# Performance work log

Hardware: AMD Instinct MI355X
Metric: run time of the kernel (lower is better)

## Reference

```python
import jax, jax.numpy as jnp
import numpy as np

NEG_SLOPE = 0.2


def gat_conv(x, edge_index, W, a_src, a_dst, b, concat):
    """PyG-style GATConv: add self-loops, linear, edge attention, scatter-softmax, scatter-add."""
    N = x.shape[0]
    H, C = a_src.shape
    loop = jnp.arange(N)
    src = jnp.concatenate([edge_index[0], loop])  # source j (messages flow j -> i)
    dst = jnp.concatenate([edge_index[1], loop])  # target i (aggregation node)
    h = (x @ W).reshape(N, H, C)                  # [N,H,C]
    alpha_s = jnp.sum(h * a_src, axis=-1)         # [N,H]
    alpha_d = jnp.sum(h * a_dst, axis=-1)         # [N,H]
    e = jax.nn.leaky_relu(alpha_s[src] + alpha_d[dst], NEG_SLOPE)  # [E,H]
    # numerically stable scatter-softmax over edges grouped by destination node
    m = jax.ops.segment_max(e, dst, num_segments=N)                # [N,H]
    ex = jnp.exp(e - m[dst])
    denom = jax.ops.segment_sum(ex, dst, num_segments=N)           # [N,H]
    alpha = ex / (denom[dst] + 1e-16)                              # [E,H]
    out = jax.ops.segment_sum(h[src] * alpha[:, :, None], dst, num_segments=N)  # [N,H,C]
    out = out.reshape(N, H * C) if concat else out.mean(axis=1)
    return out + b


def setup_inputs() -> dict:
    key = jax.random.key(0)
    ks = jax.random.split(key, 12)
    N, E, F_IN, HID, OUT, HEADS = 100000, 1600000, 128, 128, 64, 4
    C1 = HID // HEADS
    x = jax.random.normal(ks[0], (N, F_IN), dtype=jnp.float32)
    edge_index = jax.random.randint(ks[1], (2, E), 0, N, dtype=jnp.int64)
    s = 0.05
    return {
        "x": x,
        "edge_index": edge_index,
        "W1": jax.random.normal(ks[2], (F_IN, HEADS * C1), dtype=jnp.float32) * s,
        "a_src1": jax.random.normal(ks[3], (HEADS, C1), dtype=jnp.float32) * s,
        "a_dst1": jax.random.normal(ks[4], (HEADS, C1), dtype=jnp.float32) * s,
        "b1": jnp.zeros((HEADS * C1,), dtype=jnp.float32),
        "W2": jax.random.normal(ks[5], (HID, OUT), dtype=jnp.float32) * s,
        "a_src2": jax.random.normal(ks[6], (1, OUT), dtype=jnp.float32) * s,
        "a_dst2": jax.random.normal(ks[7], (1, OUT), dtype=jnp.float32) * s,
        "b2": jnp.zeros((OUT,), dtype=jnp.float32),
    }


def reference(x, edge_index, W1, a_src1, a_dst1, b1, W2, a_src2, a_dst2, b2):
    h = jax.nn.elu(gat_conv(x, edge_index, W1, a_src1, a_dst1, b1, concat=True))
    # F.dropout(p=0.5, training=False) is the identity in eval mode
    out = gat_conv(h, edge_index, W2, a_src2, a_dst2, b2, concat=False)
    return out
```

## Files before the change

### kernel.cpp

```cpp
#include <hip/hip_runtime.h>
#include <hip/hip_fp16.h>
#include <math.h>
#include <string.h>


#define BSH 9
#define DPB 512
#define NBK 256
#define CH1 16384
#define DBINS 512
#define HB 128
#define LOG2E 1.44269504088896f

using half8 = __attribute__((ext_vector_type(8))) _Float16;
using half4 = __attribute__((ext_vector_type(4))) _Float16;
using floatx4 = __attribute__((ext_vector_type(4))) float;

__device__ __forceinline__ float exp2_fast(float x) {
#if __has_builtin(__builtin_amdgcn_exp2f)
    return __builtin_amdgcn_exp2f(x);
#else
    return exp2f(x);
#endif
}

__device__ __forceinline__ void wfrag(const float* __restrict__ W, __half* __restrict__ WtF,
                                      int NC, int fid) {
    int col = fid & 15, quad = (fid >> 4) & 3, rest = fid >> 6;
    int NT = NC >> 4;
    int t = rest & (NT - 1), k0s = rest / NT;
    int n = t * 16 + col;
    int k = k0s * 32 + quad * 8;
#pragma unroll
    for (int j = 0; j < 8; ++j)
        WtF[fid * 8 + j] = __float2half(W[(k + j) * NC + n]);
}


__global__ __launch_bounds__(256) void bucket_hist(const int* __restrict__ ei, int E, int N,
                                                   unsigned* __restrict__ bcount,
                                                   const float* __restrict__ W1,
                                                   const float* __restrict__ W2,
                                                   __half* __restrict__ WtF1,
                                                   __half* __restrict__ WtF2) {
    if (blockIdx.x >= HB) {
        int tid = (blockIdx.x - HB) * 256 + threadIdx.x;
        if (tid < 2048) wfrag(W1, WtF1, 128, tid);
        else if (tid < 3072) wfrag(W2, WtF2, 64, tid - 2048);
        return;
    }
    __shared__ unsigned hist[NBK];
    int t = threadIdx.x;
    hist[t] = 0;
    __syncthreads();
    int Etot = E + N;
    for (int k = blockIdx.x * 256 + t; k < Etot; k += HB * 256) {
        int d = (k < E) ? ei[E + k] : (k - E);
        atomicAdd(&hist[d >> BSH], 1u);
    }
    __syncthreads();
    unsigned c = hist[t];
    if (c) atomicAdd(&bcount[t], c);
}

__global__ void scan_buckets(const unsigned* __restrict__ bcount, unsigned* __restrict__ bbase,
                             unsigned* __restrict__ bcursor) {
    __shared__ unsigned s[NBK];
    int t = threadIdx.x;
    unsigned v = bcount[t];
    s[t] = v;
    __syncthreads();
    for (int o = 1; o < NBK; o <<= 1) {
        unsigned add = (t >= o) ? s[t - o] : 0;
        __syncthreads();
        s[t] += add;
        __syncthreads();
    }
    unsigned excl = s[t] - v;
    bbase[t] = excl;
    bcursor[t] = excl;
    if (t == NBK - 1) bbase[NBK] = excl + v;
}

__global__ __launch_bounds__(256) void bucket_scatter(const int* __restrict__ ei, int E, int N,
                                                      unsigned* __restrict__ bcursor,
                                                      unsigned* __restrict__ rec) {
    __shared__ unsigned hist[NBK];
    __shared__ unsigned base[NBK];
    int t = threadIdx.x;
    hist[t] = 0;
    __syncthreads();
    int Etot = E + N;
    int k0 = blockIdx.x * CH1;
    int k1 = min(k0 + CH1, Etot);
    for (int k = k0 + t; k < k1; k += 256) {
        int d = (k < E) ? ei[E + k] : (k - E);
        atomicAdd(&hist[d >> BSH], 1u);
    }
    __syncthreads();
    unsigned c = hist[t];
    base[t] = c ? atomicAdd(&bcursor[t], c) : 0u;
    hist[t] = 0;
    __syncthreads();
    for (int k = k0 + t; k < k1; k += 256) {
        int s, d;
        if (k < E) { s = ei[k]; d = ei[E + k]; } else { s = d = k - E; }
        int b = d >> BSH;
        unsigned r = atomicAdd(&hist[b], 1u);
        rec[base[b] + r] = (unsigned)s | ((unsigned)(d & (DPB - 1)) << 17);
    }
}


__global__ __launch_bounds__(256) void bucket_sort(const unsigned* __restrict__ rec,
                                                   const unsigned* __restrict__ bbase,
                                                   int* __restrict__ offs, int* __restrict__ srcs,
                                                   int* __restrict__ order,
                                                   int N, int Etot) {
    __shared__ unsigned hist[DPB];
    __shared__ unsigned tsum[256];
    __shared__ unsigned deg_l[DBINS];
    int t = threadIdx.x, bb = blockIdx.x;
    unsigned r0 = bbase[bb], r1 = bbase[bb + 1];
    hist[t] = 0;
    hist[t + 256] = 0;
    deg_l[t] = 0;
    deg_l[t + 256] = 0;
    __syncthreads();
    int dlo = bb << BSH;
    for (unsigned k = r0 + t; k < r1; k += 256) {
        unsigned e = rec[k];
        atomicAdd(&hist[e >> 17], 1u);
    }
    __syncthreads();
    unsigned h0 = hist[2 * t], h1 = hist[2 * t + 1];
    int d0 = dlo + 2 * t;
    unsigned b0 = DBINS - 1u - min(h0, (unsigned)(DBINS - 1));
    unsigned b1 = DBINS - 1u - min(h1, (unsigned)(DBINS - 1));
    unsigned sub0 = 0, sub1 = 0;
    if (d0 < N) sub0 = atomicAdd(&deg_l[b0], 1u);
    if (d0 + 1 < N) sub1 = atomicAdd(&deg_l[b1], 1u);
    tsum[t] = h0 + h1;
    __syncthreads();
    for (int o = 1; o < 256; o <<= 1) {
        unsigned a = (t >= o) ? tsum[t - o] : 0;
        __syncthreads();
        tsum[t] += a;
        __syncthreads();
    }
    unsigned tb = tsum[t] - (h0 + h1);
    if (d0 < N) offs[d0] = (int)(r0 + tb);
    if (d0 + 1 < N) offs[d0 + 1] = (int)(r0 + tb + h0);
    hist[2 * t] = tb;
    hist[2 * t + 1] = tb + h0;
    __syncthreads();
    for (unsigned k = r0 + t; k < r1; k += 256) {
        unsigned e = rec[k];
        unsigned r = atomicAdd(&hist[e >> 17], 1u);
        srcs[r0 + r] = (int)(e & 0x1FFFFu);
    }
    if (bb == 0 && t == 0) offs[N] = Etot;
    __syncthreads();
    unsigned c0 = deg_l[t], c1 = deg_l[t + 256];
    hist[t] = c0;
    hist[t + 256] = c1;
    __syncthreads();
    for (int o = 1; o < DBINS; o <<= 1) {
        unsigned a0 = (t >= o) ? deg_l[t - o] : 0u;
        unsigned a1 = (t + 256 >= o) ? deg_l[t + 256 - o] : 0u;
        __syncthreads();
        deg_l[t] += a0;
        deg_l[t + 256] += a1;
        __syncthreads();
    }
    int NFULL = N >> BSH;
    unsigned TAIL = (unsigned)(N - (NFULL << BSH));
    if (d0 < N) {
        unsigned r = deg_l[b0] - hist[b0] + sub0;
        order[(int)(r * (unsigned)NFULL + min(r, TAIL)) + bb] = d0;
    }
    if (d0 + 1 < N) {
        unsigned r = deg_l[b1] - hist[b1] + sub1;
        order[(int)(r * (unsigned)NFULL + min(r, TAIL)) + bb] = d0 + 1;
    }
}


template <int NC, int H, typename InT>
__global__ __launch_bounds__(256) void gemm_mfma(const InT* __restrict__ A,
                                                 const __half* __restrict__ WtF,
                                                 __half* __restrict__ C,
                                                 const float* __restrict__ a_src,
                                                 const float* __restrict__ a_dst,
                                                 float* __restrict__ as,
                                                 float* __restrict__ ad, int M) {
    constexpr int NT = NC / 16;
    constexpr int TPH = NT / H;
    int wave = threadIdx.x >> 6;
    int lane = threadIdx.x & 63;
    int quad = lane >> 4, col = lane & 15;
    int row0 = blockIdx.x * 64 + wave * 16;
    int arow = row0 + col;
    if (arow >= M) arow = M - 1;
    floatx4 acc[NT] = {};
    const half8* wf = reinterpret_cast<const half8*>(WtF) + lane;
#pragma unroll
    for (int k0s = 0; k0s < 4; ++k0s) {
        int k0 = k0s * 32;
        half8 af;
        if constexpr (sizeof(InT) == 4) {
            const float* ap = (const float*)A + (size_t)arow * 128 + k0 + quad * 8;
            float4 v0 = *reinterpret_cast<const float4*>(ap);
            float4 v1 = *reinterpret_cast<const float4*>(ap + 4);
            af[0] = (_Float16)v0.x; af[1] = (_Float16)v0.y;
            af[2] = (_Float16)v0.z; af[3] = (_Float16)v0.w;
            af[4] = (_Float16)v1.x; af[5] = (_Float16)v1.y;
            af[6] = (_Float16)v1.z; af[7] = (_Float16)v1.w;
        } else {
            af = *reinterpret_cast<const half8*>((const __half*)A + (size_t)arow * 128 + k0 + quad * 8);
        }
#pragma unroll
        for (int t = 0; t < NT; ++t) {
            half8 bf = wf[(k0s * NT + t) * 64];
            acc[t] = __builtin_amdgcn_mfma_f32_16x16x32_f16(af, bf, acc[t], 0, 0, 0);
        }
    }
    float sa[NT], da[NT];
#pragma unroll
    for (int t = 0; t < NT; ++t) {
        sa[t] = a_src[t * 16 + col];
        da[t] = a_dst[t * 16 + col];
    }
    int rbase = row0 + quad * 4;
#pragma unroll
    for (int reg = 0; reg < 4; ++reg) {
        int row = rbase + reg;
        bool live = row < M;
        if (live) {
#pragma unroll
            for (int t = 0; t < NT; ++t)
                C[(size_t)row * NC + t * 16 + col] = __float2half(acc[t][reg]);
        }
#pragma unroll
        for (int h = 0; h < H; ++h) {
            float ps = 0.f, pd = 0.f;
#pragma unroll
            for (int tt = 0; tt < TPH; ++tt) {
                int t = h * TPH + tt;
                ps = fmaf(acc[t][reg], sa[t], ps);
                pd = fmaf(acc[t][reg], da[t], pd);
            }
#pragma unroll
            for (int o = 1; o < 16; o <<= 1) {
                ps += __shfl_xor(ps, o, 64);
                pd += __shfl_xor(pd, o, 64);
            }
            if (col == 0 && live) {
                as[(size_t)row * H + h] = ps * LOG2E;
                ad[(size_t)row * H + h] = pd * LOG2E;
            }
        }
    }
}


template <int CPL>
__device__ __forceinline__ void ldrow(const __half* __restrict__ p, _Float16* f) {
    if constexpr (CPL == 8) {
        half8 v = *reinterpret_cast<const half8*>(p);
#pragma unroll
        for (int c = 0; c < 8; ++c) f[c] = v[c];
    } else {
        half4 v = *reinterpret_cast<const half4*>(p);
#pragma unroll
        for (int c = 0; c < 4; ++c) f[c] = v[c];
    }
}

template <int H, int ROWS, int CW, bool DOELU, typename OutT>
__global__ __launch_bounds__(256) void aggregateQ(const __half* __restrict__ h,
                                                  const float* __restrict__ as,
                                                  const float* __restrict__ ad,
                                                  const int* __restrict__ offs,
                                                  const int* __restrict__ srcs,
                                                  const int* __restrict__ order,
                                                  const float* __restrict__ bias,
                                                  OutT* __restrict__ out, int N) {
    constexpr int CPL = CW / 16;
    unsigned wave = (blockIdx.x * blockDim.x + threadIdx.x) >> 6;
    unsigned lane = threadIdx.x & 63;
    unsigned lig = lane & 15;
    unsigned idx = wave * 4u + (lane >> 4);
    bool live = idx < (unsigned)N;
    unsigned nc = (unsigned)order[live ? idx : 0u];
    unsigned chan = lig * CPL;
    unsigned head = (chan * H) / ROWS;
    float adv = ad[nc * H + head];
    int e0 = offs[nc], e1 = offs[nc + 1];
    int deg = e1 - e0, e1m1 = e1 - 1;
    int md = deg;
    md = max(md, __shfl_xor(md, 16, 64));
    md = max(md, __shfl_xor(md, 32, 64));
    float accs[CPL] = {};
    float den = 0.f;
    for (int k = 0; k < md; k += 4) {
        int b = e0 + k;
        unsigned j0 = (unsigned)srcs[min(b, e1m1)];
        unsigned j1 = (unsigned)srcs[min(b + 1, e1m1)];
        unsigned j2 = (unsigned)srcs[min(b + 2, e1m1)];
        unsigned j3 = (unsigned)srcs[min(b + 3, e1m1)];
        float t0 = as[j0 * H + head] + adv;
        float t1 = as[j1 * H + head] + adv;
        float t2 = as[j2 * H + head] + adv;
        float t3 = as[j3 * H + head] + adv;
        _Float16 f0[CPL], f1[CPL], f2[CPL], f3[CPL];
        ldrow<CPL>(h + j0 * (unsigned)ROWS + chan, f0);
        ldrow<CPL>(h + j1 * (unsigned)ROWS + chan, f1);
        ldrow<CPL>(h + j2 * (unsigned)ROWS + chan, f2);
        ldrow<CPL>(h + j3 * (unsigned)ROWS + chan, f3);
        float x0 = exp2_fast(fmaxf(t0, 0.2f * t0));
        float x1 = exp2_fast(fmaxf(t1, 0.2f * t1));
        float x2 = exp2_fast(fmaxf(t2, 0.2f * t2));
        float x3 = exp2_fast(fmaxf(t3, 0.2f * t3));
        x0 = (k < deg) ? x0 : 0.f;
        x1 = (k + 1 < deg) ? x1 : 0.f;
        x2 = (k + 2 < deg) ? x2 : 0.f;
        x3 = (k + 3 < deg) ? x3 : 0.f;
#pragma unroll
        for (int c = 0; c < CPL; ++c) accs[c] = fmaf(x0, (float)f0[c], accs[c]);
#pragma unroll
        for (int c = 0; c < CPL; ++c) accs[c] = fmaf(x1, (float)f1[c], accs[c]);
#pragma unroll
        for (int c = 0; c < CPL; ++c) accs[c] = fmaf(x2, (float)f2[c], accs[c]);
#pragma unroll
        for (int c = 0; c < CPL; ++c) accs[c] = fmaf(x3, (float)f3[c], accs[c]);
        den += x0 + x1;
        den += x2 + x3;
    }
    float r = 1.0f / (den + 1e-16f);
    if (!live) return;
    const float* bp = bias + chan;
    float vs[CPL];
#pragma unroll
    for (int c = 0; c < CPL; ++c) {
        float v = accs[c] * r + bp[c];
        if constexpr (DOELU) v = (v > 0.f) ? v : expm1f(v);
        vs[c] = v;
    }
    if constexpr (sizeof(OutT) == 2) {
        __half2 st[CPL / 2];
#pragma unroll
        for (int q = 0; q < CPL / 2; ++q)
            st[q] = __floats2half2_rn(vs[2 * q], vs[2 * q + 1]);
        if constexpr (CPL == 8) {
            uint4 v; memcpy(&v, st, 16);
            *reinterpret_cast<uint4*>((__half*)out + nc * (unsigned)ROWS + chan) = v;
        } else {
            uint2 v; memcpy(&v, st, 8);
            *reinterpret_cast<uint2*>((__half*)out + nc * (unsigned)ROWS + chan) = v;
        }
    } else {
#pragma unroll
        for (int q4 = 0; q4 < CPL; q4 += 4) {
            float4 v = make_float4(vs[q4], vs[q4 + 1], vs[q4 + 2], vs[q4 + 3]);
            *reinterpret_cast<float4*>((float*)out + nc * (unsigned)ROWS + chan + q4) = v;
        }
    }
}


extern "C" void kernel_launch(void* const* d_in, const int* in_sizes, int n_in,
                              void* d_out, int out_size, void* d_ws, size_t ws_size,
                              hipStream_t stream) {
    const float* x      = (const float*)d_in[0];
    const int*   ei     = (const int*)d_in[1];
    const float* W1     = (const float*)d_in[2];
    const float* a_src1 = (const float*)d_in[3];
    const float* a_dst1 = (const float*)d_in[4];
    const float* b1     = (const float*)d_in[5];
    const float* W2     = (const float*)d_in[6];
    const float* a_src2 = (const float*)d_in[7];
    const float* a_dst2 = (const float*)d_in[8];
    const float* b2     = (const float*)d_in[9];
    float* out = (float*)d_out;

    const int N = out_size / 64;
    const int E = in_sizes[1] / 2;
    const int Etot = E + N;

    size_t off = 0;
    auto carve = [&](size_t bytes) -> void* {
        void* p = (char*)d_ws + off;
        off += (bytes + 255) & ~(size_t)255;
        return p;
    };
    __half* h1      = (__half*)carve((size_t)N * 128 * 2);
    __half* hmid    = (__half*)carve((size_t)N * 128 * 2);
    float* as1      = (float*)carve((size_t)N * 4 * 4);
    float* ad1      = (float*)carve((size_t)N * 4 * 4);
    float* as2      = (float*)carve((size_t)N * 4);
    float* ad2      = (float*)carve((size_t)N * 4);
    int*   offs     = (int*)carve((size_t)(N + 1) * 4);
    int*   srcs     = (int*)carve((size_t)Etot * 4);
    unsigned* rec   = (unsigned*)carve((size_t)Etot * 4);
    int*   order    = (int*)carve((size_t)N * 4);
    unsigned* bcount  = (unsigned*)carve(NBK * 4);
    unsigned* bbase   = (unsigned*)carve((NBK + 1) * 4);
    unsigned* bcursor = (unsigned*)carve(NBK * 4);
    __half* WtF1    = (__half*)carve(128 * 128 * 2);
    __half* WtF2    = (__half*)carve(64 * 128 * 2);
    __half* h2      = h1;

    const int NSB = (N + DPB - 1) / DPB;
    const int GB  = (N + 63) / 64;

    hipMemsetAsync(bcount, 0, NBK * sizeof(unsigned), stream);
    bucket_hist<<<HB + 12, 256, 0, stream>>>(ei, E, N, bcount, W1, W2, WtF1, WtF2);
    scan_buckets<<<1, 256, 0, stream>>>(bcount, bbase, bcursor);
    bucket_scatter<<<(Etot + CH1 - 1) / CH1, 256, 0, stream>>>(ei, E, N, bcursor, rec);
    bucket_sort<<<NSB, 256, 0, stream>>>(rec, bbase, offs, srcs, order, N, Etot);

    gemm_mfma<128, 4, float><<<GB, 256, 0, stream>>>(
        x, WtF1, h1, a_src1, a_dst1, as1, ad1, N);
    aggregateQ<4, 128, 128, true, __half><<<(N + 15) / 16, 256, 0, stream>>>(
        h1, as1, ad1, offs, srcs, order, b1, hmid, N);

    gemm_mfma<64, 1, __half><<<GB, 256, 0, stream>>>(
        hmid, WtF2, h2, a_src2, a_dst2, as2, ad2, N);
    aggregateQ<1, 64, 64, false, float><<<(N + 15) / 16, 256, 0, stream>>>(
        h2, as2, ad2, offs, srcs, order, b2, out, N);
}
```

Baseline: 350.6 us.

## Fuse layer-1 aggregation with layer-2 linear transform and attention logits

Replaces the layer-1 aggregation kernel plus the second MFMA GEMM with one kernel. Each block aggregates 16 destination nodes, applies bias and ELU into shared memory, then multiplies by a pre-rearranged fp16 W2 with scalar FMAs and computes the layer-2 attention logits. This removes the round trip of the 128-wide hidden activation through global memory and one kernel launch. In exchange, the layer-2 matmul moves from MFMA to scalar fp32 FMAs, with a block-wide sync and heavier register and shared-memory use in the aggregation kernel.

```diff
diff --git a/kernel.cpp b/kernel.cpp
--- a/kernel.cpp
+++ b/kernel.cpp
@@ -36,17 +36,25 @@
         WtF[fid * 8 + j] = __float2half(W[(k + j) * NC + n]);
 }
 
+__device__ __forceinline__ void wfrag2(const float* __restrict__ W2, __half* __restrict__ W2g,
+                                       int fid) {
+    int o = fid & 63, cc = fid >> 6;
+#pragma unroll
+    for (int j = 0; j < 8; ++j)
+        W2g[fid * 8 + j] = __float2half(W2[(cc * 8 + j) * 64 + o]);
+}
+
 
 __global__ __launch_bounds__(256) void bucket_hist(const int* __restrict__ ei, int E, int N,
                                                    unsigned* __restrict__ bcount,
                                                    const float* __restrict__ W1,
                                                    const float* __restrict__ W2,
                                                    __half* __restrict__ WtF1,
-                                                   __half* __restrict__ WtF2) {
+                                                   __half* __restrict__ W2g) {
     if (blockIdx.x >= HB) {
         int tid = (blockIdx.x - HB) * 256 + threadIdx.x;
         if (tid < 2048) wfrag(W1, WtF1, 128, tid);
-        else if (tid < 3072) wfrag(W2, WtF2, 64, tid - 2048);
+        else if (tid < 3072) wfrag2(W2, W2g, tid - 2048);
         return;
     }
     __shared__ unsigned hist[NBK];
@@ -259,6 +267,131 @@
                 as[(size_t)row * H + h] = ps * LOG2E;
                 ad[(size_t)row * H + h] = pd * LOG2E;
             }
+        }
+    }
+}
+
+
+__global__ __launch_bounds__(256) void aggregate1F(const __half* __restrict__ h,
+                                                   const float* __restrict__ as,
+                                                   const float* __restrict__ ad,
+                                                   const int* __restrict__ offs,
+                                                   const int* __restrict__ srcs,
+                                                   const int* __restrict__ order,
+                                                   const float* __restrict__ bias,
+                                                   const __half* __restrict__ W2g,
+                                                   const float* __restrict__ a_src2,
+                                                   const float* __restrict__ a_dst2,
+                                                   __half* __restrict__ h2,
+                                                   float* __restrict__ as2,
+                                                   float* __restrict__ ad2, int N) {
+    constexpr int CPL = 8, H = 4, ROWS = 128;
+    __shared__ float hm[16][128];
+    unsigned wave = (blockIdx.x * blockDim.x + threadIdx.x) >> 6;
+    unsigned lane = threadIdx.x & 63;
+    unsigned lig = lane & 15;
+    unsigned g = lane >> 4;
+    unsigned idx = wave * 4u + g;
+    bool live = idx < (unsigned)N;
+    unsigned nc = (unsigned)order[live ? idx : 0u];
+    unsigned chan = lig * CPL;
+    unsigned head = (chan * H) / ROWS;
+    float adv = ad[nc * H + head];
+    int e0 = offs[nc], e1 = offs[nc + 1];
+    int deg = e1 - e0, e1m1 = e1 - 1;
+    int md = deg;
+    md = max(md, __shfl_xor(md, 16, 64));
+    md = max(md, __shfl_xor(md, 32, 64));
+    float accs[CPL] = {};
+    float den = 0.f;
+    for (int k = 0; k < md; k += 4) {
+        int b = e0 + k;
+        unsigned j0 = (unsigned)srcs[min(b, e1m1)];
+        unsigned j1 = (unsigned)srcs[min(b + 1, e1m1)];
+        unsigned j2 = (unsigned)srcs[min(b + 2, e1m1)];
+        unsigned j3 = (unsigned)srcs[min(b + 3, e1m1)];
+        float t0 = as[j0 * H + head] + adv;
+        float t1 = as[j1 * H + head] + adv;
+        float t2 = as[j2 * H + head] + adv;
+        float t3 = as[j3 * H + head] + adv;
+        _Float16 f0[CPL], f1[CPL], f2[CPL], f3[CPL];
+        {
+            half8 v0 = *reinterpret_cast<const half8*>(h + j0 * (unsigned)ROWS + chan);
+            half8 v1 = *reinterpret_cast<const half8*>(h + j1 * (unsigned)ROWS + chan);
+            half8 v2 = *reinterpret_cast<const half8*>(h + j2 * (unsigned)ROWS + chan);
+            half8 v3 = *reinterpret_cast<const half8*>(h + j3 * (unsigned)ROWS + chan);
+#pragma unroll
+            for (int c = 0; c < CPL; ++c) { f0[c] = v0[c]; f1[c] = v1[c]; f2[c] = v2[c]; f3[c] = v3[c]; }
+        }
+        float x0 = exp2_fast(fmaxf(t0, 0.2f * t0));
+        float x1 = exp2_fast(fmaxf(t1, 0.2f * t1));
+        float x2 = exp2_fast(fmaxf(t2, 0.2f * t2));
+        float x3 = exp2_fast(fmaxf(t3, 0.2f * t3));
+        x0 = (k < deg) ? x0 : 0.f;
+        x1 = (k + 1 < deg) ? x1 : 0.f;
+        x2 = (k + 2 < deg) ? x2 : 0.f;
+        x3 = (k + 3 < deg) ? x3 : 0.f;
+#pragma unroll
+        for (int c = 0; c < CPL; ++c) accs[c] = fmaf(x0, (float)f0[c], accs[c]);
+#pragma unroll
+        for (int c = 0; c < CPL; ++c) accs[c] = fmaf(x1, (float)f1[c], accs[c]);
+#pragma unroll
+        for (int c = 0; c < CPL; ++c) accs[c] = fmaf(x2, (float)f2[c], accs[c]);
+#pragma unroll
+        for (int c = 0; c < CPL; ++c) accs[c] = fmaf(x3, (float)f3[c], accs[c]);
+        den += x0 + x1;
+        den += x2 + x3;
+    }
+    float r = 1.0f / (den + 1e-16f);
+    unsigned w_in_b = threadIdx.x >> 6;
+    unsigned nib = w_in_b * 4 + g;
+    const float* bp = bias + chan;
+#pragma unroll
+    for (int c = 0; c < CPL; ++c) {
+        float v = accs[c] * r + bp[c];
+        v = (v > 0.f) ? v : expm1f(v);
+        hm[nib][chan + c] = v;
+    }
+    __syncthreads();
+    int o = (int)lane;
+    float ag[4] = {0.f, 0.f, 0.f, 0.f};
+    const half8* wg = reinterpret_cast<const half8*>(W2g);
+    int wb = (int)w_in_b * 4;
+#pragma unroll
+    for (int cc = 0; cc < 16; ++cc) {
+        half8 w = wg[cc * 64 + o];
+        float wf[8];
+#pragma unroll
+        for (int j = 0; j < 8; ++j) wf[j] = (float)w[j];
+#pragma unroll
+        for (int gg = 0; gg < 4; ++gg) {
+            const floatx4* hp = reinterpret_cast<const floatx4*>(&hm[wb + gg][cc * 8]);
+            floatx4 a = hp[0], b2v = hp[1];
+            ag[gg] = fmaf(a[0], wf[0], ag[gg]);
+            ag[gg] = fmaf(a[1], wf[1], ag[gg]);
+            ag[gg] = fmaf(a[2], wf[2], ag[gg]);
+            ag[gg] = fmaf(a[3], wf[3], ag[gg]);
+            ag[gg] = fmaf(b2v[0], wf[4], ag[gg]);
+            ag[gg] = fmaf(b2v[1], wf[5], ag[gg]);
+            ag[gg] = fmaf(b2v[2], wf[6], ag[gg]);
+            ag[gg] = fmaf(b2v[3], wf[7], ag[gg]);
+        }
+    }
+    float s2 = a_src2[o], d2 = a_dst2[o];
+#pragma unroll
+    for (int gg = 0; gg < 4; ++gg) {
+        float hv = ag[gg];
+        float ps = hv * s2, pd = hv * d2;
+#pragma unroll
+        for (int off = 1; off < 64; off <<= 1) {
+            ps += __shfl_xor(ps, off, 64);
+            pd += __shfl_xor(pd, off, 64);
+        }
+        bool glive = (wave * 4u + (unsigned)gg) < (unsigned)N;
+        unsigned ng = (unsigned)__shfl((int)nc, gg * 16, 64);
+        if (glive) {
+            h2[ng * 64u + (unsigned)o] = __float2half(hv);
+            if (lane == 0) { as2[ng] = ps * LOG2E; ad2[ng] = pd * LOG2E; }
         }
     }
 }
@@ -395,7 +528,7 @@
         return p;
     };
     __half* h1      = (__half*)carve((size_t)N * 128 * 2);
-    __half* hmid    = (__half*)carve((size_t)N * 128 * 2);
+    __half* h2      = (__half*)carve((size_t)N * 64 * 2);
     float* as1      = (float*)carve((size_t)N * 4 * 4);
     float* ad1      = (float*)carve((size_t)N * 4 * 4);
     float* as2      = (float*)carve((size_t)N * 4);
@@ -408,25 +541,22 @@
     unsigned* bbase   = (unsigned*)carve((NBK + 1) * 4);
     unsigned* bcursor = (unsigned*)carve(NBK * 4);
     __half* WtF1    = (__half*)carve(128 * 128 * 2);
-    __half* WtF2    = (__half*)carve(64 * 128 * 2);
-    __half* h2      = h1;
+    __half* W2g     = (__half*)carve(64 * 128 * 2);
 
     const int NSB = (N + DPB - 1) / DPB;
     const int GB  = (N + 63) / 64;
 
     hipMemsetAsync(bcount, 0, NBK * sizeof(unsigned), stream);
-    bucket_hist<<<HB + 12, 256, 0, stream>>>(ei, E, N, bcount, W1, W2, WtF1, WtF2);
+    bucket_hist<<<HB + 12, 256, 0, stream>>>(ei, E, N, bcount, W1, W2, WtF1, W2g);
     scan_buckets<<<1, 256, 0, stream>>>(bcount, bbase, bcursor);
     bucket_scatter<<<(Etot + CH1 - 1) / CH1, 256, 0, stream>>>(ei, E, N, bcursor, rec);
     bucket_sort<<<NSB, 256, 0, stream>>>(rec, bbase, offs, srcs, order, N, Etot);
 
     gemm_mfma<128, 4, float><<<GB, 256, 0, stream>>>(
         x, WtF1, h1, a_src1, a_dst1, as1, ad1, N);
-    aggregateQ<4, 128, 128, true, __half><<<(N + 15) / 16, 256, 0, stream>>>(
-        h1, as1, ad1, offs, srcs, order, b1, hmid, N);
-
-    gemm_mfma<64, 1, __half><<<GB, 256, 0, stream>>>(
-        hmid, WtF2, h2, a_src2, a_dst2, as2, ad2, N);
+    aggregate1F<<<(N + 15) / 16, 256, 0, stream>>>(
+        h1, as1, ad1, offs, srcs, order, b1, W2g, a_src2, a_dst2, h2, as2, ad2, N);
+
     aggregateQ<1, 64, 64, false, float><<<(N + 15) / 16, 256, 0, stream>>>(
         h2, as2, ad2, offs, srcs, order, b2, out, N);
 }
```

After: 645.5 us. 84.1% more time.
